# Optimization experiments

Hardware: AMD Instinct MI355X
Metric: run time of the kernel (lower is better)

The kernel has to match this reference:

```python
import jax, jax.numpy as jnp
import numpy as np

B, CIN, D = 16, 2, 64
COUT, K = 13, 5

def setup_inputs() -> dict:
    key = jax.random.key(0)
    kx, kw, kb = jax.random.split(key, 3)
    x = jax.random.normal(kx, (B, CIN, D, D, D), dtype=jnp.float32)
    # 13 branches of Conv3d(2,1,5) fused: stacked weights [13,2,5,5,5], bias [13]
    fan_in = CIN * K * K * K
    bound = 1.0 / np.sqrt(fan_in)
    W = jax.random.uniform(kw, (COUT, CIN, K, K, K), jnp.float32, -bound, bound)
    b = jax.random.uniform(kb, (COUT,), jnp.float32, -bound, bound)
    return {"x": x, "W": W, "b": b}

def reference(x, W, b):
    # fused equivalent of 13 parallel Conv3d(2->1,k=5,'same') + concat
    y = jax.lax.conv_general_dilated(
        x, W,
        window_strides=(1, 1, 1),
        padding='SAME',
        dimension_numbers=('NCDHW', 'OIDHW', 'NCDHW'))
    y = y + b[None, :, None, None, None]
    return jnp.clip(y, 0.0, 100.0)
```

## Files before the change

### kernel.cpp

```cpp
#include <hip/hip_runtime.h>


typedef __attribute__((ext_vector_type(8))) short bf16x8;
typedef __attribute__((ext_vector_type(4))) float f32x4;
typedef unsigned short u16;

#define YB 8
#define YR 12
#define ROWB 144
#define SLOTB 2048
#define CIB 16384
#define ZSTEPS 8

#define PZ 68
#define PY 68
#define P_PLANE (PY * ROWB)
#define P_BYTES ((size_t)16 * 2 * PZ * P_PLANE)

__device__ __forceinline__ unsigned f2bf(float f) {
    unsigned u = __builtin_bit_cast(unsigned, f);
    return (u + 0x7FFFu + ((u >> 16) & 1u)) >> 16;
}

__global__ __launch_bounds__(256)
void pad_bf16(const float* __restrict__ X, u16* __restrict__ P) {
    int idx = blockIdx.x * 256 + threadIdx.x;
    int q = idx % 18;
    int r = idx / 18;
    int yp = r % 68; r /= 68;
    int zp = r % 68; r /= 68;
    int ci = r & 1;
    int b  = r >> 1;
    int z = zp - 2, y = yp - 2;
    bool rowok = ((unsigned)z < 64u) && ((unsigned)y < 64u);
    const float* src = X + ((((size_t)b * 2 + ci) * 64 + z) * 64 + y) * 64;
    u16 h[4];
    #pragma unroll
    for (int j = 0; j < 4; ++j) {
        int x = 4 * q + j - 2;
        float v = (rowok && (unsigned)x < 64u) ? src[x] : 0.0f;
        h[j] = (u16)f2bf(v);
    }
    *(ushort4*)(P + (size_t)idx * 4) = make_ushort4(h[0], h[1], h[2], h[3]);
}

__device__ __forceinline__ void gl16(const void* g, void* l) {
    __builtin_amdgcn_global_load_lds(
        (const __attribute__((address_space(1))) void*)g,
        (__attribute__((address_space(3))) void*)l, 16, 0, 0);
}

__global__ __launch_bounds__(256, 1)
void conv13_async(const u16* __restrict__ P, const float* __restrict__ W,
                  const float* __restrict__ Bv, float* __restrict__ O) {
    __shared__ char lds[2 * CIB];

    const int tid = threadIdx.x;
    const int l   = tid & 63;
    const int wid = tid >> 6;
    const int g   = l >> 4;
    const int lx  = l & 15;
    const int yt = blockIdx.x;
    const int zc = blockIdx.y;
    const int b  = blockIdx.z;
    const int zlo = zc * 16;
    const int yp0 = yt * YB;
    const int zz  = wid >> 1;
    const int yy0 = (wid & 1) * 4;

    unsigned wf[13][4];
    int cOff[13], dzv[13];
    #pragma unroll
    for (int s = 0; s < 13; ++s) {
        int r  = 4 * s + g;
        int rc = (r < 50) ? r : 49;
        int ci = rc / 25, r2 = rc % 25, dz = r2 / 5, dy = r2 % 5;
        dzv[s]  = dz;
        cOff[s] = ci * CIB + (yy0 + dy) * ROWB + 8 * lx;
        float w0 = 0.f, w1 = 0.f, w2 = 0.f, w3 = 0.f, w4 = 0.f;
        if (lx < 13 && r < 50) {
            const float* wr = W + ((lx * 2 + ci) * 25 + dz * 5 + dy) * 5;
            w0 = wr[0]; w1 = wr[1]; w2 = wr[2]; w3 = wr[3]; w4 = wr[4];
        }
        wf[s][0] = f2bf(w0) | (f2bf(w1) << 16);
        wf[s][1] = f2bf(w2) | (f2bf(w3) << 16);
        wf[s][2] = f2bf(w4);
        wf[s][3] = 0u;
    }
    float bvv[4];
    #pragma unroll
    for (int v = 0; v < 4; ++v) {
        int co = 4 * g + v;
        bvv[v] = (co < 13) ? Bv[co] : 0.0f;
    }

    const char* Pc = (const char*)P;
    int c1 = 64 + l; if (c1 > 107) c1 = 107;

    for (int r = wid; r < 12; r += 4) {
        int ci = r / 6, pl = r % 6;
        const char* gb = Pc + (((size_t)(b * 2 + ci) * PZ + (zlo + pl)) * P_PLANE)
                            + (size_t)yp0 * ROWB;
        char* lb = lds + ci * CIB + pl * SLOTB;
        gl16(gb + 16 * l,  lb);
        gl16(gb + 16 * c1, lb + 1024);
    }
    __syncthreads();

    #pragma unroll 1
    for (int t = 0; t < ZSTEPS; ++t) {
        if (t < ZSTEPS - 1) {
            int ci = wid >> 1, pl = wid & 1;
            int slot = (2 * t + 6 + pl) & 7;
            int zp = zlo + 2 * t + 6 + pl;
            const char* gb = Pc + (((size_t)(b * 2 + ci) * PZ + zp) * P_PLANE)
                                + (size_t)yp0 * ROWB;
            char* lb = lds + ci * CIB + slot * SLOTB;
            gl16(gb + 16 * l,  lb);
            gl16(gb + 16 * c1, lb + 1024);
        }

        const int uw = 2 * t + zz;
        f32x4 acc[4][4];
        #pragma unroll
        for (int i = 0; i < 4; ++i)
            #pragma unroll
            for (int sh = 0; sh < 4; ++sh)
                acc[i][sh] = (f32x4){ bvv[0], bvv[1], bvv[2], bvv[3] };

        #pragma unroll
        for (int s = 0; s < 13; ++s) {
            int ab = cOff[s] + (((uw + dzv[s]) & 7) * SLOTB);
            bf16x8 bb[4];
            #pragma unroll
            for (int i = 0; i < 4; ++i) {
                const char* p = lds + ab + i * ROWB;
                uint2 lo = *(const uint2*)p;
                uint2 hi = *(const uint2*)(p + 8);
                union { unsigned u[4]; bf16x8 v; } tmp;
                tmp.u[0] = lo.x; tmp.u[1] = lo.y; tmp.u[2] = hi.x; tmp.u[3] = hi.y;
                bb[i] = tmp.v;
            }
            unsigned a0 = wf[s][0], a1 = wf[s][1], a2 = wf[s][2], a3 = wf[s][3];
            #pragma unroll
            for (int sh = 0; sh < 4; ++sh) {
                if (sh) {
                    unsigned n1 = (a1 << 16) | (a0 >> 16);
                    unsigned n2 = (a2 << 16) | (a1 >> 16);
                    unsigned n3 = (a3 << 16) | (a2 >> 16);
                    a0 <<= 16; a1 = n1; a2 = n2; a3 = n3;
                }
                union { unsigned u[4]; bf16x8 v; } av;
                av.u[0] = a0; av.u[1] = a1; av.u[2] = a2; av.u[3] = a3;
                #pragma unroll
                for (int i = 0; i < 4; ++i)
                    acc[i][sh] = __builtin_amdgcn_mfma_f32_16x16x32_bf16(av.v, bb[i], acc[i][sh], 0, 0, 0);
            }
        }

        const int oz = zlo + 2 * t + zz;
        #pragma unroll
        for (int i = 0; i < 4; ++i) {
            int oy = yt * YB + yy0 + i;
            float* dst = O + (size_t)b * 3407872 + oz * 4096 + oy * 64 + 4 * lx;
            #pragma unroll
            for (int v = 0; v < 4; ++v) {
                int co = 4 * g + v;
                if (co < 13) {
                    f32x4 o4 = { fminf(fmaxf(acc[i][0][v], 0.0f), 100.0f),
                                 fminf(fmaxf(acc[i][1][v], 0.0f), 100.0f),
                                 fminf(fmaxf(acc[i][2][v], 0.0f), 100.0f),
                                 fminf(fmaxf(acc[i][3][v], 0.0f), 100.0f) };
                    *(f32x4*)(dst + (size_t)co * 262144) = o4;
                }
            }
        }

        __syncthreads();
    }
}

#define F_YR 12
#define F_UPITCH 72
#define F_ROWB 144

__global__ __launch_bounds__(256, 2)
void conv13_mfma_shift(const float* __restrict__ X,
                       const float* __restrict__ W,
                       const float* __restrict__ Bv,
                       float* __restrict__ O) {
    __shared__ unsigned short lds[144 * F_UPITCH];

    const int tid = threadIdx.x;
    const int l   = tid & 63;
    const int wid = tid >> 6;
    const int g   = l >> 4;
    const int lx  = l & 15;
    const int yt = blockIdx.x, zt = blockIdx.y, b = blockIdx.z;

    unsigned wf[13][4];
    int rowConst[13];
    #pragma unroll
    for (int s = 0; s < 13; ++s) {
        int r  = 4 * s + g;
        int rc = (r < 50) ? r : 49;
        int ci = rc / 25, r2 = rc % 25, dz = r2 / 5, dy = r2 % 5;
        rowConst[s] = (ci * 72 + dz * F_YR + dy) * F_ROWB;
        float w0 = 0.f, w1 = 0.f, w2 = 0.f, w3 = 0.f, w4 = 0.f;
        if (lx < 13 && r < 50) {
            const float* wr = W + ((lx * 2 + ci) * 25 + dz * 5 + dy) * 5;
            w0 = wr[0]; w1 = wr[1]; w2 = wr[2]; w3 = wr[3]; w4 = wr[4];
        }
        wf[s][0] = f2bf(w0) | (f2bf(w1) << 16);
        wf[s][1] = f2bf(w2) | (f2bf(w3) << 16);
        wf[s][2] = f2bf(w4);
        wf[s][3] = 0u;
    }

    const int gz0 = zt * 2 - 2, gy0 = yt * 8 - 2;
    for (int idx = tid; idx < 144 * 18; idx += 256) {
        int row = idx / 18, q = idx % 18;
        int ci = row / 72;
        int rz = (row / F_YR) % 6;
        int ry = row % F_YR;
        int zi = gz0 + rz, yi = gy0 + ry;
        float v0 = 0.f, v1 = 0.f, v2 = 0.f, v3 = 0.f;
        if ((unsigned)zi < 64u && (unsigned)yi < 64u) {
            const float* src = X + ((((size_t)b * 2 + ci) * 64 + zi) * 64 + yi) * 64;
            int x0 = 4 * q - 2;
            if ((unsigned)(x0 + 0) < 64u) v0 = src[x0 + 0];
            if ((unsigned)(x0 + 1) < 64u) v1 = src[x0 + 1];
            if ((unsigned)(x0 + 2) < 64u) v2 = src[x0 + 2];
            if ((unsigned)(x0 + 3) < 64u) v3 = src[x0 + 3];
        }
        unsigned* lp = (unsigned*)&lds[row * F_UPITCH + 4 * q];
        lp[0] = f2bf(v0) | (f2bf(v1) << 16);
        lp[1] = f2bf(v2) | (f2bf(v3) << 16);
    }

    int tileOff[4], ozv[4], oyv[4];
    #pragma unroll
    for (int i = 0; i < 4; ++i) {
        int t = wid * 4 + i, zz = t >> 3, yy = t & 7;
        tileOff[i] = (zz * F_YR + yy) * F_ROWB;
        ozv[i] = zt * 2 + zz;
        oyv[i] = yt * 8 + yy;
    }
    float bvv[4];
    #pragma unroll
    for (int v = 0; v < 4; ++v) {
        int co = 4 * g + v;
        bvv[v] = (co < 13) ? Bv[co] : 0.0f;
    }
    f32x4 acc[4][4];
    #pragma unroll
    for (int i = 0; i < 4; ++i)
        #pragma unroll
        for (int sh = 0; sh < 4; ++sh)
            acc[i][sh] = (f32x4){ bvv[0], bvv[1], bvv[2], bvv[3] };
    __syncthreads();

    #pragma unroll
    for (int s = 0; s < 13; ++s) {
        bf16x8 bb[4];
        #pragma unroll
        for (int i = 0; i < 4; ++i) {
            const char* p = (const char*)lds + (rowConst[s] + tileOff[i] + 8 * lx);
            uint2 lo = *(const uint2*)p;
            uint2 hi = *(const uint2*)(p + 8);
            union { unsigned u[4]; bf16x8 v; } tmp;
            tmp.u[0] = lo.x; tmp.u[1] = lo.y; tmp.u[2] = hi.x; tmp.u[3] = hi.y;
            bb[i] = tmp.v;
        }
        unsigned a0 = wf[s][0], a1 = wf[s][1], a2 = wf[s][2], a3 = wf[s][3];
        #pragma unroll
        for (int sh = 0; sh < 4; ++sh) {
            if (sh) {
                unsigned n1 = (a1 << 16) | (a0 >> 16);
                unsigned n2 = (a2 << 16) | (a1 >> 16);
                unsigned n3 = (a3 << 16) | (a2 >> 16);
                a0 <<= 16; a1 = n1; a2 = n2; a3 = n3;
            }
            union { unsigned u[4]; bf16x8 v; } av;
            av.u[0] = a0; av.u[1] = a1; av.u[2] = a2; av.u[3] = a3;
            #pragma unroll
            for (int i = 0; i < 4; ++i)
                acc[i][sh] = __builtin_amdgcn_mfma_f32_16x16x32_bf16(av.v, bb[i], acc[i][sh], 0, 0, 0);
        }
    }
    #pragma unroll
    for (int i = 0; i < 4; ++i) {
        float* dst = O + ((((size_t)b * 13) * 64 + ozv[i]) * 64 + oyv[i]) * 64 + 4 * lx;
        #pragma unroll
        for (int v = 0; v < 4; ++v) {
            int co = 4 * g + v;
            if (co < 13) {
                f32x4 o4 = { fminf(fmaxf(acc[i][0][v], 0.0f), 100.0f),
                             fminf(fmaxf(acc[i][1][v], 0.0f), 100.0f),
                             fminf(fmaxf(acc[i][2][v], 0.0f), 100.0f),
                             fminf(fmaxf(acc[i][3][v], 0.0f), 100.0f) };
                *(f32x4*)(dst + (size_t)co * 262144) = o4;
            }
        }
    }
}

extern "C" void kernel_launch(void* const* d_in, const int* in_sizes, int n_in,
                              void* d_out, int out_size, void* d_ws, size_t ws_size,
                              hipStream_t stream) {
    const float* X  = (const float*)d_in[0];
    const float* W  = (const float*)d_in[1];
    const float* Bv = (const float*)d_in[2];
    float* O = (float*)d_out;

    if (ws_size >= P_BYTES) {
        u16* P = (u16*)d_ws;
        pad_bf16<<<10404, 256, 0, stream>>>(X, P);
        conv13_async<<<dim3(8, 4, 16), 256, 0, stream>>>(P, W, Bv, O);
    } else {
        conv13_mfma_shift<<<dim3(8, 32, 16), 256, 0, stream>>>(X, W, Bv, O);
    }
}
```

Baseline: 75.98 us.

## Cut register pressure to allow two blocks per CU and double z-chunk grid

Restructures the MFMA loop so accumulators are kept for one output row at a time (4 f32x4 instead of 16), packs the dz offset into the column offset, and drops a zero weight register. This lowers VGPR use enough to request two blocks per CU via launch bounds. ZSTEPS is halved and the grid doubled in z, giving 1024 blocks instead of 512 for better occupancy and latency hiding. In exchange, each LDS B-fragment is now loaded once per weight row rather than being reused across rows, and every block pays the prologue (weight conversion, initial 6-plane loads) over fewer steps.

```diff
diff --git a/kernel.cpp b/kernel.cpp
--- a/kernel.cpp
+++ b/kernel.cpp
@@ -10,7 +10,7 @@
 #define ROWB 144
 #define SLOTB 2048
 #define CIB 16384
-#define ZSTEPS 8
+#define ZSTEPS 4
 
 #define PZ 68
 #define PY 68
@@ -50,7 +50,7 @@
         (__attribute__((address_space(3))) void*)l, 16, 0, 0);
 }
 
-__global__ __launch_bounds__(256, 1)
+__global__ __launch_bounds__(256, 2)
 void conv13_async(const u16* __restrict__ P, const float* __restrict__ W,
                   const float* __restrict__ Bv, float* __restrict__ O) {
     __shared__ char lds[2 * CIB];
@@ -63,20 +63,19 @@
     const int yt = blockIdx.x;
     const int zc = blockIdx.y;
     const int b  = blockIdx.z;
-    const int zlo = zc * 16;
+    const int zlo = zc * (2 * ZSTEPS);
     const int yp0 = yt * YB;
     const int zz  = wid >> 1;
     const int yy0 = (wid & 1) * 4;
 
-    unsigned wf[13][4];
-    int cOff[13], dzv[13];
+    unsigned wf[13][3];
+    int cOffD[13];
     #pragma unroll
     for (int s = 0; s < 13; ++s) {
         int r  = 4 * s + g;
         int rc = (r < 50) ? r : 49;
         int ci = rc / 25, r2 = rc % 25, dz = r2 / 5, dy = r2 % 5;
-        dzv[s]  = dz;
-        cOff[s] = ci * CIB + (yy0 + dy) * ROWB + 8 * lx;
+        cOffD[s] = (ci * CIB + (yy0 + dy) * ROWB + 8 * lx) | dz;
         float w0 = 0.f, w1 = 0.f, w2 = 0.f, w3 = 0.f, w4 = 0.f;
         if (lx < 13 && r < 50) {
             const float* wr = W + ((lx * 2 + ci) * 25 + dz * 5 + dy) * 5;
@@ -85,7 +84,6 @@
         wf[s][0] = f2bf(w0) | (f2bf(w1) << 16);
         wf[s][1] = f2bf(w2) | (f2bf(w3) << 16);
         wf[s][2] = f2bf(w4);
-        wf[s][3] = 0u;
     }
     float bvv[4];
     #pragma unroll
@@ -121,56 +119,50 @@
         }
 
         const int uw = 2 * t + zz;
-        f32x4 acc[4][4];
-        #pragma unroll
-        for (int i = 0; i < 4; ++i)
+        const int oz = zlo + uw;
+        #pragma unroll
+        for (int i = 0; i < 4; ++i) {
+            f32x4 acc[4];
             #pragma unroll
             for (int sh = 0; sh < 4; ++sh)
-                acc[i][sh] = (f32x4){ bvv[0], bvv[1], bvv[2], bvv[3] };
-
-        #pragma unroll
-        for (int s = 0; s < 13; ++s) {
-            int ab = cOff[s] + (((uw + dzv[s]) & 7) * SLOTB);
-            bf16x8 bb[4];
+                acc[sh] = (f32x4){ bvv[0], bvv[1], bvv[2], bvv[3] };
+
             #pragma unroll
-            for (int i = 0; i < 4; ++i) {
-                const char* p = lds + ab + i * ROWB;
+            for (int s = 0; s < 13; ++s) {
+                int cD = cOffD[s];
+                int dz = cD & 7;
+                int ab = (cD ^ dz) + (((uw + dz) & 7) * SLOTB) + i * ROWB;
+                const char* p = lds + ab;
                 uint2 lo = *(const uint2*)p;
                 uint2 hi = *(const uint2*)(p + 8);
-                union { unsigned u[4]; bf16x8 v; } tmp;
-                tmp.u[0] = lo.x; tmp.u[1] = lo.y; tmp.u[2] = hi.x; tmp.u[3] = hi.y;
-                bb[i] = tmp.v;
+                union { unsigned u[4]; bf16x8 v; } bbv;
+                bbv.u[0] = lo.x; bbv.u[1] = lo.y; bbv.u[2] = hi.x; bbv.u[3] = hi.y;
+
+                unsigned a0 = wf[s][0], a1 = wf[s][1], a2 = wf[s][2], a3 = 0u;
+                #pragma unroll
+                for (int sh = 0; sh < 4; ++sh) {
+                    if (sh) {
+                        unsigned n1 = (a1 << 16) | (a0 >> 16);
+                        unsigned n2 = (a2 << 16) | (a1 >> 16);
+                        unsigned n3 = (a3 << 16) | (a2 >> 16);
+                        a0 <<= 16; a1 = n1; a2 = n2; a3 = n3;
+                    }
+                    union { unsigned u[4]; bf16x8 v; } av;
+                    av.u[0] = a0; av.u[1] = a1; av.u[2] = a2; av.u[3] = a3;
+                    acc[sh] = __builtin_amdgcn_mfma_f32_16x16x32_bf16(av.v, bbv.v, acc[sh], 0, 0, 0);
+                }
             }
-            unsigned a0 = wf[s][0], a1 = wf[s][1], a2 = wf[s][2], a3 = wf[s][3];
-            #pragma unroll
-            for (int sh = 0; sh < 4; ++sh) {
-                if (sh) {
-                    unsigned n1 = (a1 << 16) | (a0 >> 16);
-                    unsigned n2 = (a2 << 16) | (a1 >> 16);
-                    unsigned n3 = (a3 << 16) | (a2 >> 16);
-                    a0 <<= 16; a1 = n1; a2 = n2; a3 = n3;
-                }
-                union { unsigned u[4]; bf16x8 v; } av;
-                av.u[0] = a0; av.u[1] = a1; av.u[2] = a2; av.u[3] = a3;
-                #pragma unroll
-                for (int i = 0; i < 4; ++i)
-                    acc[i][sh] = __builtin_amdgcn_mfma_f32_16x16x32_bf16(av.v, bb[i], acc[i][sh], 0, 0, 0);
-            }
-        }
-
-        const int oz = zlo + 2 * t + zz;
-        #pragma unroll
-        for (int i = 0; i < 4; ++i) {
+
             int oy = yt * YB + yy0 + i;
             float* dst = O + (size_t)b * 3407872 + oz * 4096 + oy * 64 + 4 * lx;
             #pragma unroll
             for (int v = 0; v < 4; ++v) {
                 int co = 4 * g + v;
                 if (co < 13) {
-                    f32x4 o4 = { fminf(fmaxf(acc[i][0][v], 0.0f), 100.0f),
-                                 fminf(fmaxf(acc[i][1][v], 0.0f), 100.0f),
-                                 fminf(fmaxf(acc[i][2][v], 0.0f), 100.0f),
-                                 fminf(fmaxf(acc[i][3][v], 0.0f), 100.0f) };
+                    f32x4 o4 = { fminf(fmaxf(acc[0][v], 0.0f), 100.0f),
+                                 fminf(fmaxf(acc[1][v], 0.0f), 100.0f),
+                                 fminf(fmaxf(acc[2][v], 0.0f), 100.0f),
+                                 fminf(fmaxf(acc[3][v], 0.0f), 100.0f) };
                     *(f32x4*)(dst + (size_t)co * 262144) = o4;
                 }
             }
@@ -316,7 +308,7 @@
     if (ws_size >= P_BYTES) {
         u16* P = (u16*)d_ws;
         pad_bf16<<<10404, 256, 0, stream>>>(X, P);
-        conv13_async<<<dim3(8, 4, 16), 256, 0, stream>>>(P, W, Bv, O);
+        conv13_async<<<dim3(8, 8, 16), 256, 0, stream>>>(P, W, Bv, O);
     } else {
         conv13_mfma_shift<<<dim3(8, 32, 16), 256, 0, stream>>>(X, W, Bv, O);
     }
```

After: 137.7 us. +81.3%, slower.
